# Optimization experiments

Hardware: AMD Instinct MI355X
Metric: run time of the kernel (lower is better)

## Reference

```python
import jax, jax.numpy as jnp
import numpy as np

L, B, N, D = 512, 8, 32, 256
GH, AH = 128, 64  # gate hidden, attn hidden


def setup_inputs() -> dict:
    key = jax.random.key(0)
    ks = jax.random.split(key, 11)
    s = lambda fan_in: 1.0 / np.sqrt(fan_in)
    return {
        "vert_feat": jax.random.normal(ks[0], (L, B, N, D), jnp.float32),
        "horiz_feat": jax.random.normal(ks[1], (L, B, N, D), jnp.float32),
        "mask_BNL": jax.random.bernoulli(ks[2], 0.5, (B, N, L)),
        "gw1": jax.random.uniform(ks[3], (GH, 2 * D), jnp.float32, -s(2 * D), s(2 * D)),
        "gb1": jax.random.uniform(ks[4], (GH,), jnp.float32, -s(2 * D), s(2 * D)),
        "gw2": jax.random.uniform(ks[5], (1, GH), jnp.float32, -s(GH), s(GH)),
        "gb2": jax.random.uniform(ks[6], (1,), jnp.float32, -s(GH), s(GH)),
        "aw1": jax.random.uniform(ks[7], (AH, D), jnp.float32, -s(D), s(D)),
        "ab1": jax.random.uniform(ks[8], (AH,), jnp.float32, -s(D), s(D)),
        "aw2": jax.random.uniform(ks[9], (1, AH), jnp.float32, -s(AH), s(AH)),
        "ab2": jax.random.uniform(ks[10], (1,), jnp.float32, -s(AH), s(AH)),
    }


def reference(vert_feat, horiz_feat, mask_BNL, gw1, gb1, gw2, gb2, aw1, ab1, aw2, ab2):
    # gate MLP on concat features: [L,B,N,2D] -> [L,B,N,1]
    comb = jnp.concatenate([vert_feat, horiz_feat], axis=-1)
    h = jax.nn.relu(comb @ gw1.T + gb1)
    gate = jax.nn.sigmoid(h @ gw2.T + gb2)  # [L,B,N,1]
    per_msg = gate * vert_feat + (1.0 - gate) * horiz_feat  # [L,B,N,D]
    # scorer MLP -> logits [L,B,N]
    a = jnp.tanh(per_msg @ aw1.T + ab1)
    logits = (a @ aw2.T + ab2)[..., 0]  # [L,B,N]
    logits_BLN = jnp.transpose(logits, (1, 0, 2))  # [B,L,N]
    mask_BLN = jnp.transpose(mask_BNL, (0, 2, 1))  # [B,L,N]
    logits_BLN = jnp.where(mask_BLN, logits_BLN, -jnp.inf)
    attn = jax.nn.softmax(logits_BLN, axis=-1)
    attn = jnp.nan_to_num(attn, nan=0.0)  # rows fully masked -> 0
    # weighted sum over messages: per_msg as [B,L,N,D]
    fused_BLD = jnp.einsum("bln,lbnd->bld", attn, per_msg)
    fused = jnp.transpose(fused_BLD, (1, 0, 2))  # [L,B,D]
    return fused, per_msg, attn
```

## Files before the change

kernel.cpp:

```cpp
#include <hip/hip_runtime.h>
#include <hip/hip_bf16.h>
#include <math.h>

#define LL 512
#define BB 8
#define NN 32
#define DD 256
#define GH 128
#define AH 64

#define PA 520
#define PW1 136
#define PW2 264

typedef short short8 __attribute__((ext_vector_type(8)));
typedef float f32x4  __attribute__((ext_vector_type(4)));

__device__ __forceinline__ float bf2f(unsigned short u) {
  return __uint_as_float(((unsigned int)u) << 16);
}
__device__ __forceinline__ unsigned short f2bf(float f) {
  union { __hip_bfloat16 h; unsigned short u; } cv;
  cv.h = __float2bfloat16(f);
  return cv.u;
}

extern "C" __global__ __launch_bounds__(256, 2)
void dynfusion_kernel(const float* __restrict__ vert,
                      const float* __restrict__ horiz,
                      const int*   __restrict__ mask,
                      const float* __restrict__ gw1,
                      const float* __restrict__ gb1,
                      const float* __restrict__ gw2,
                      const float* __restrict__ gb2,
                      const float* __restrict__ aw1,
                      const float* __restrict__ ab1,
                      const float* __restrict__ aw2,
                      const float* __restrict__ ab2,
                      float* __restrict__ out)
{
  __shared__ __align__(16) unsigned short sA[NN * PA];
  __shared__ __align__(16) unsigned short sW[GH * PW1];
  __shared__ float sPart[NN][2];
  __shared__ float sGb1R[GH], sGw2R[GH];
  __shared__ float sAb1R[AH], sAw2R[AH];
  __shared__ float sGate[NN], sAttn[NN], sScal[2];

  const int t  = threadIdx.x;
  const int lb = blockIdx.x;
  const int l  = lb >> 3;
  const int b  = lb & 7;
  const size_t msgBase = (size_t)lb * NN * DD;

  const int lane = t & 63;
  const int w    = t >> 6;
  const int lr   = lane & 15;
  const int lg   = lane >> 4;
  const int mt   = w & 1;
  const int ns   = (w >> 1) << 6;
  const int js   = (w >> 1) << 5;
  const int aoff = (mt * 16 + lr) * PA;

  float* __restrict__ outF  = out;
  float* __restrict__ outPM = out + 1048576;
  float* __restrict__ outAT = out + 34603008;

  if (t < GH) { sGb1R[t] = gb1[t]; sGw2R[t] = gw2[t]; }
  if (t < AH) { sAb1R[t] = ab1[t]; sAw2R[t] = aw2[t]; }
  if (t == 0) { sScal[0] = gb2[0]; sScal[1] = ab2[0]; }

#pragma unroll
  for (int i = 0; i < 16; ++i) {
    int idx4 = i * 256 + t;
    int n  = idx4 >> 7;
    int c4 = (idx4 & 127) << 2;
    const float* src = (c4 < DD) ? (vert  + msgBase + n * DD + c4)
                                 : (horiz + msgBase + n * DD + (c4 - DD));
    float4 v4 = *reinterpret_cast<const float4*>(src);
    ushort4 pk;
    pk.x = f2bf(v4.x); pk.y = f2bf(v4.y); pk.z = f2bf(v4.z); pk.w = f2bf(v4.w);
    *reinterpret_cast<ushort4*>(&sA[n * PA + c4]) = pk;
  }

  f32x4 acc1[4] = {};
  for (int kc = 0; kc < 4; ++kc) {
    __syncthreads();
#pragma unroll
    for (int i = 0; i < 16; ++i) {
      int idx4 = i * 256 + t;
      int j  = idx4 >> 5;
      int k4 = (idx4 & 31) << 2;
      float4 wv = *reinterpret_cast<const float4*>(gw1 + j * 512 + kc * 128 + k4);
      ushort4 pk;
      pk.x = f2bf(wv.x); pk.y = f2bf(wv.y); pk.z = f2bf(wv.z); pk.w = f2bf(wv.w);
      *reinterpret_cast<ushort4*>(&sW[j * PW1 + k4]) = pk;
    }
    __syncthreads();
#pragma unroll
    for (int ks = 0; ks < 4; ++ks) {
      short8 af = *reinterpret_cast<const short8*>(&sA[aoff + kc * 128 + ks * 32 + lg * 8]);
#pragma unroll
      for (int nt = 0; nt < 4; ++nt) {
        short8 bf = *reinterpret_cast<const short8*>(&sW[(ns + nt * 16 + lr) * PW1 + ks * 32 + lg * 8]);
        acc1[nt] = __builtin_amdgcn_mfma_f32_16x16x32_bf16(af, bf, acc1[nt], 0, 0, 0);
      }
    }
  }

  {
    float p[4] = {0.f, 0.f, 0.f, 0.f};
#pragma unroll
    for (int nt = 0; nt < 4; ++nt) {
      int j = ns + nt * 16 + lr;
      float bj = sGb1R[j], wj = sGw2R[j];
#pragma unroll
      for (int r = 0; r < 4; ++r) {
        float hv = fmaxf(acc1[nt][r] + bj, 0.0f);
        p[r] += hv * wj;
      }
    }
#pragma unroll
    for (int msk = 1; msk <= 8; msk <<= 1)
#pragma unroll
      for (int r = 0; r < 4; ++r) p[r] += __shfl_xor(p[r], msk);
    if (lr == 0) {
#pragma unroll
      for (int r = 0; r < 4; ++r) sPart[mt * 16 + lg * 4 + r][w >> 1] = p[r];
    }
  }
  __syncthreads();
  if (t < NN) {
    float sv = sScal[0] + sPart[t][0] + sPart[t][1];
    sGate[t] = 1.0f / (1.0f + __expf(-sv));
  }
  __syncthreads();

#pragma unroll
  for (int i = 0; i < 8; ++i) {
    int idx4 = i * 256 + t;
    int n  = idx4 >> 6;
    int d0 = (idx4 & 63) << 2;
    float g = sGate[n];
    ushort4 vq = *reinterpret_cast<const ushort4*>(&sA[n * PA + d0]);
    ushort4 hq = *reinterpret_cast<const ushort4*>(&sA[n * PA + DD + d0]);
    float4 pr;
    pr.x = bf2f(hq.x) + g * (bf2f(vq.x) - bf2f(hq.x));
    pr.y = bf2f(hq.y) + g * (bf2f(vq.y) - bf2f(hq.y));
    pr.z = bf2f(hq.z) + g * (bf2f(vq.z) - bf2f(hq.z));
    pr.w = bf2f(hq.w) + g * (bf2f(vq.w) - bf2f(hq.w));
    ushort4 pq;
    pq.x = f2bf(pr.x); pq.y = f2bf(pr.y); pq.z = f2bf(pr.z); pq.w = f2bf(pr.w);
    *reinterpret_cast<ushort4*>(&sA[n * PA + d0]) = pq;
    *reinterpret_cast<float4*>(outPM + msgBase + n * DD + d0) = pr;
  }
  __syncthreads();

#pragma unroll
  for (int i = 0; i < 16; ++i) {
    int idx4 = i * 256 + t;
    int j  = idx4 >> 6;
    int k4 = (idx4 & 63) << 2;
    float4 wv = *reinterpret_cast<const float4*>(aw1 + j * 256 + k4);
    ushort4 pk;
    pk.x = f2bf(wv.x); pk.y = f2bf(wv.y); pk.z = f2bf(wv.z); pk.w = f2bf(wv.w);
    *reinterpret_cast<ushort4*>(&sW[j * PW2 + k4]) = pk;
  }
  __syncthreads();

  f32x4 acc2[2] = {};
#pragma unroll
  for (int ks = 0; ks < 8; ++ks) {
    short8 af = *reinterpret_cast<const short8*>(&sA[aoff + ks * 32 + lg * 8]);
#pragma unroll
    for (int q = 0; q < 2; ++q) {
      short8 bf = *reinterpret_cast<const short8*>(&sW[(js + q * 16 + lr) * PW2 + ks * 32 + lg * 8]);
      acc2[q] = __builtin_amdgcn_mfma_f32_16x16x32_bf16(af, bf, acc2[q], 0, 0, 0);
    }
  }

  {
    float p[4] = {0.f, 0.f, 0.f, 0.f};
#pragma unroll
    for (int q = 0; q < 2; ++q) {
      int j = js + q * 16 + lr;
      float bj = sAb1R[j], wj = sAw2R[j];
#pragma unroll
      for (int r = 0; r < 4; ++r) {
        float av = tanhf(acc2[q][r] + bj);
        p[r] += av * wj;
      }
    }
#pragma unroll
    for (int msk = 1; msk <= 8; msk <<= 1)
#pragma unroll
      for (int r = 0; r < 4; ++r) p[r] += __shfl_xor(p[r], msk);
    if (lr == 0) {
#pragma unroll
      for (int r = 0; r < 4; ++r) sPart[mt * 16 + lg * 4 + r][w >> 1] = p[r];
    }
  }
  __syncthreads();

  if (t < 64) {
    float logit = -INFINITY;
    bool valid = false;
    if (t < 32) {
      float sv = sScal[1] + sPart[t][0] + sPart[t][1];
      valid = (mask[((size_t)b * NN + t) * LL + l] != 0);
      logit = valid ? sv : -INFINITY;
    }
    float m = logit;
#pragma unroll
    for (int off = 32; off >= 1; off >>= 1) m = fmaxf(m, __shfl_xor(m, off));
    float e = (valid && m > -INFINITY) ? __expf(logit - m) : 0.0f;
    float ssum = e;
#pragma unroll
    for (int off = 32; off >= 1; off >>= 1) ssum += __shfl_xor(ssum, off);
    float at = (ssum > 0.0f) ? (e / ssum) : 0.0f;
    if (t < 32) {
      sAttn[t] = at;
      outAT[((size_t)b * LL + l) * NN + t] = at;
    }
  }
  __syncthreads();

  {
    int d = t;
    float f = 0.0f;
#pragma unroll
    for (int n = 0; n < NN; ++n) f += sAttn[n] * bf2f(sA[n * PA + d]);
    outF[(size_t)lb * DD + d] = f;
  }
}

extern "C" void kernel_launch(void* const* d_in, const int* in_sizes, int n_in,
                              void* d_out, int out_size, void* d_ws, size_t ws_size,
                              hipStream_t stream) {
  dynfusion_kernel<<<dim3(LL * BB), dim3(256), 0, stream>>>(
      (const float*)d_in[0],
      (const float*)d_in[1],
      (const int*)d_in[2],
      (const float*)d_in[3],
      (const float*)d_in[4],
      (const float*)d_in[5],
      (const float*)d_in[6],
      (const float*)d_in[7],
      (const float*)d_in[8],
      (const float*)d_in[9],
      (const float*)d_in[10],
      (float*)d_out);
}
```

Before: 400.6 us.

## Pre-convert weights to bf16 in tiled layout and stream MFMA B-operands from global

Adds a small pre-kernel that converts gw1 and aw1 to bf16 in a k-blocked layout in the workspace, run on every call. The main kernel then reads MFMA B fragments straight from global/L2 instead of having each of the 4096 blocks convert and stage the weights through shared memory. This removes the shared weight buffer and several syncthreads, allowing the occupancy hint to go from 2 to 4 blocks per CU. The mask load is also hoisted to kernel start. In exchange it adds a second launch and relies on L2 hit rates for the repeated weight reads.

Result: faster. 389.2 us (-2.8%).

```diff
diff --git a/kernel.cpp b/kernel.cpp
--- a/kernel.cpp
+++ b/kernel.cpp
@@ -10,8 +10,6 @@
 #define AH 64
 
 #define PA 520
-#define PW1 136
-#define PW2 264
 
 typedef short short8 __attribute__((ext_vector_type(8)));
 typedef float f32x4  __attribute__((ext_vector_type(4)));
@@ -25,22 +23,35 @@
   return cv.u;
 }
 
-extern "C" __global__ __launch_bounds__(256, 2)
+extern "C" __global__ void wconv(const float* __restrict__ gw1,
+                                 const float* __restrict__ aw1,
+                                 unsigned short* __restrict__ ws)
+{
+  int o = blockIdx.x * 256 + threadIdx.x;
+  if (o < 65536) {
+    int kb = o >> 12, r = o & 4095, j = r >> 5, ko = r & 31;
+    ws[o] = f2bf(gw1[j * 512 + kb * 32 + ko]);
+  } else {
+    int o2 = o - 65536;
+    int kb = o2 >> 11, j = (o2 >> 5) & 63, ko = o2 & 31;
+    ws[o] = f2bf(aw1[j * 256 + kb * 32 + ko]);
+  }
+}
+
+extern "C" __global__ __launch_bounds__(256, 4)
 void dynfusion_kernel(const float* __restrict__ vert,
                       const float* __restrict__ horiz,
                       const int*   __restrict__ mask,
-                      const float* __restrict__ gw1,
                       const float* __restrict__ gb1,
                       const float* __restrict__ gw2,
                       const float* __restrict__ gb2,
-                      const float* __restrict__ aw1,
                       const float* __restrict__ ab1,
                       const float* __restrict__ aw2,
                       const float* __restrict__ ab2,
+                      const unsigned short* __restrict__ ws,
                       float* __restrict__ out)
 {
   __shared__ __align__(16) unsigned short sA[NN * PA];
-  __shared__ __align__(16) unsigned short sW[GH * PW1];
   __shared__ float sPart[NN][2];
   __shared__ float sGb1R[GH], sGw2R[GH];
   __shared__ float sAb1R[AH], sAw2R[AH];
@@ -61,9 +72,15 @@
   const int js   = (w >> 1) << 5;
   const int aoff = (mt * 16 + lr) * PA;
 
+  const unsigned short* __restrict__ gw1t = ws;
+  const unsigned short* __restrict__ aw1t = ws + 65536;
+
   float* __restrict__ outF  = out;
   float* __restrict__ outPM = out + 1048576;
   float* __restrict__ outAT = out + 34603008;
+
+  int mval = 0;
+  if (t < NN) mval = mask[((size_t)b * NN + t) * LL + l];
 
   if (t < GH) { sGb1R[t] = gb1[t]; sGw2R[t] = gw2[t]; }
   if (t < AH) { sAb1R[t] = ab1[t]; sAw2R[t] = aw2[t]; }
@@ -81,27 +98,17 @@
     pk.x = f2bf(v4.x); pk.y = f2bf(v4.y); pk.z = f2bf(v4.z); pk.w = f2bf(v4.w);
     *reinterpret_cast<ushort4*>(&sA[n * PA + c4]) = pk;
   }
+  __syncthreads();
 
   f32x4 acc1[4] = {};
-  for (int kc = 0; kc < 4; ++kc) {
-    __syncthreads();
-#pragma unroll
-    for (int i = 0; i < 16; ++i) {
-      int idx4 = i * 256 + t;
-      int j  = idx4 >> 5;
-      int k4 = (idx4 & 31) << 2;
-      float4 wv = *reinterpret_cast<const float4*>(gw1 + j * 512 + kc * 128 + k4);
-      ushort4 pk;
-      pk.x = f2bf(wv.x); pk.y = f2bf(wv.y); pk.z = f2bf(wv.z); pk.w = f2bf(wv.w);
-      *reinterpret_cast<ushort4*>(&sW[j * PW1 + k4]) = pk;
-    }
-    __syncthreads();
-#pragma unroll
-    for (int ks = 0; ks < 4; ++ks) {
-      short8 af = *reinterpret_cast<const short8*>(&sA[aoff + kc * 128 + ks * 32 + lg * 8]);
+  {
+    const unsigned short* bgp = gw1t + (ns + lr) * 32 + lg * 8;
+#pragma unroll
+    for (int ks = 0; ks < 16; ++ks) {
+      short8 af = *reinterpret_cast<const short8*>(&sA[aoff + ks * 32 + lg * 8]);
 #pragma unroll
       for (int nt = 0; nt < 4; ++nt) {
-        short8 bf = *reinterpret_cast<const short8*>(&sW[(ns + nt * 16 + lr) * PW1 + ks * 32 + lg * 8]);
+        short8 bf = *reinterpret_cast<const short8*>(bgp + ks * 4096 + nt * 512);
         acc1[nt] = __builtin_amdgcn_mfma_f32_16x16x32_bf16(af, bf, acc1[nt], 0, 0, 0);
       }
     }
@@ -155,26 +162,17 @@
   }
   __syncthreads();
 
-#pragma unroll
-  for (int i = 0; i < 16; ++i) {
-    int idx4 = i * 256 + t;
-    int j  = idx4 >> 6;
-    int k4 = (idx4 & 63) << 2;
-    float4 wv = *reinterpret_cast<const float4*>(aw1 + j * 256 + k4);
-    ushort4 pk;
-    pk.x = f2bf(wv.x); pk.y = f2bf(wv.y); pk.z = f2bf(wv.z); pk.w = f2bf(wv.w);
-    *reinterpret_cast<ushort4*>(&sW[j * PW2 + k4]) = pk;
-  }
-  __syncthreads();
-
   f32x4 acc2[2] = {};
-#pragma unroll
-  for (int ks = 0; ks < 8; ++ks) {
-    short8 af = *reinterpret_cast<const short8*>(&sA[aoff + ks * 32 + lg * 8]);
-#pragma unroll
-    for (int q = 0; q < 2; ++q) {
-      short8 bf = *reinterpret_cast<const short8*>(&sW[(js + q * 16 + lr) * PW2 + ks * 32 + lg * 8]);
-      acc2[q] = __builtin_amdgcn_mfma_f32_16x16x32_bf16(af, bf, acc2[q], 0, 0, 0);
+  {
+    const unsigned short* bap = aw1t + (js + lr) * 32 + lg * 8;
+#pragma unroll
+    for (int ks = 0; ks < 8; ++ks) {
+      short8 af = *reinterpret_cast<const short8*>(&sA[aoff + ks * 32 + lg * 8]);
+#pragma unroll
+      for (int q = 0; q < 2; ++q) {
+        short8 bf = *reinterpret_cast<const short8*>(bap + ks * 2048 + q * 512);
+        acc2[q] = __builtin_amdgcn_mfma_f32_16x16x32_bf16(af, bf, acc2[q], 0, 0, 0);
+      }
     }
   }
 
@@ -206,7 +204,7 @@
     bool valid = false;
     if (t < 32) {
       float sv = sScal[1] + sPart[t][0] + sPart[t][1];
-      valid = (mask[((size_t)b * NN + t) * LL + l] != 0);
+      valid = (mval != 0);
       logit = valid ? sv : -INFINITY;
     }
     float m = logit;
@@ -236,17 +234,21 @@
 extern "C" void kernel_launch(void* const* d_in, const int* in_sizes, int n_in,
                               void* d_out, int out_size, void* d_ws, size_t ws_size,
                               hipStream_t stream) {
+  wconv<<<dim3(320), dim3(256), 0, stream>>>(
+      (const float*)d_in[3],
+      (const float*)d_in[7],
+      (unsigned short*)d_ws);
+
   dynfusion_kernel<<<dim3(LL * BB), dim3(256), 0, stream>>>(
       (const float*)d_in[0],
       (const float*)d_in[1],
       (const int*)d_in[2],
-      (const float*)d_in[3],
       (const float*)d_in[4],
       (const float*)d_in[5],
       (const float*)d_in[6],
-      (const float*)d_in[7],
       (const float*)d_in[8],
       (const float*)d_in[9],
       (const float*)d_in[10],
+      (const unsigned short*)d_ws,
       (float*)d_out);
 }
```
